# Kernel tuning notes

Hardware: AMD Instinct MI355X
Metric: run time of the kernel (lower is better)

The kernel has to match this reference:

```python
import jax, jax.numpy as jnp
import numpy as np

EPSILON = 0.1
GAMMA = 1.0
STOPERR = 1e-06
NUM_ITER_MAX = 1000


def setup_inputs() -> dict:
    key = jax.random.key(0)
    P = jax.random.uniform(key, (65536, 1024), dtype=jnp.float32)
    return {"P": P}


def _sinkhorn_scalings(Q, Pa, Pb, fi):
    # Iterate b <- (Pb / (Q^T a))^fi with a = Pa / (Q b); device-side convergence check.
    K = Q.shape[1]
    b0 = jnp.full((K, 1), 1.0 / K, dtype=Q.dtype)
    a0 = jnp.zeros((Q.shape[0], 1), dtype=Q.dtype)  # overwritten on first iter

    def cond(state):
        a, b, err, it = state
        return jnp.logical_and(err > STOPERR, it < NUM_ITER_MAX)

    def body(state):
        _, b, _, it = state
        a = Pa / jnp.maximum(Q @ b, 1e-12)            # (N,1)
        b_new = (Pb / jnp.maximum(Q.T @ a, 1e-12)) ** fi  # (K,1)
        err = jnp.linalg.norm(b_new - b)
        return (a, b_new, err, it + 1)

    a, b, _, _ = jax.lax.while_loop(
        cond, body, (a0, b0, jnp.float32(1.0), jnp.int32(0)))
    return a, b


def reference(P):
    N, K = P.shape
    eps = max(EPSILON, 1e-08)
    Q = jnp.maximum(jnp.exp(-P / eps), 1e-12)          # (N,K)
    Pa = jnp.full((N, 1), 1.0 / N, dtype=P.dtype)
    Pb = jnp.full((K, 1), 1.0 / K, dtype=P.dtype)
    fi = GAMMA / (GAMMA + eps)

    a, b = _sinkhorn_scalings(Q, Pa, Pb, fi)

    OT_plan = N * a * Q * b.T                          # (N,K)
    ot_loss = jnp.mean(jnp.sum(OT_plan * P, axis=1))
    w = jnp.mean(OT_plan, axis=0, keepdims=True)       # (1,K)
    w = w / (jnp.sum(w, axis=1, keepdims=True) + 1e-08)
    # F.kl_div(log(w+1e-7), Pb_row, reduction='batchmean'), batch size = 1:
    Pb_row = Pb.reshape(1, -1)
    reg = jnp.sum(Pb_row * (jnp.log(Pb_row) - jnp.log(w + 1e-07)))
    return (OT_plan, ot_loss, reg)
```

## Files before the change

### kernel.cpp

```cpp
#include <hip/hip_runtime.h>
#include <hip/hip_cooperative_groups.h>

constexpr int   NROWS = 65536;
constexpr int   NK    = 1024;
constexpr float PAv   = 1.0f / 65536.0f;
constexpr float PBv   = 1.0f / 1024.0f;
constexpr float FI    = 1.0f / 1.1f;
constexpr float NEG_INV_EPS = -10.0f;
constexpr float STOPERR2 = 1e-12f;
constexpr int   MAXIT = 1000;
constexpr float INVS  = 1.0f / 65535.0f;

__global__ __launch_bounds__(256)
void q_conv_kernel(const float* __restrict__ P, uint4* __restrict__ Qb)
{
  const size_t total8 = (size_t)NROWS * NK / 8;
  for (size_t i = (size_t)blockIdx.x * blockDim.x + threadIdx.x; i < total8;
       i += (size_t)gridDim.x * blockDim.x) {
    const float4* p4 = reinterpret_cast<const float4*>(P) + 2 * i;
    float4 a = p4[0], b = p4[1];
    unsigned int u0 = __float2uint_rn(__expf(a.x * NEG_INV_EPS) * 65535.0f);
    unsigned int u1 = __float2uint_rn(__expf(a.y * NEG_INV_EPS) * 65535.0f);
    unsigned int u2 = __float2uint_rn(__expf(a.z * NEG_INV_EPS) * 65535.0f);
    unsigned int u3 = __float2uint_rn(__expf(a.w * NEG_INV_EPS) * 65535.0f);
    unsigned int u4 = __float2uint_rn(__expf(b.x * NEG_INV_EPS) * 65535.0f);
    unsigned int u5 = __float2uint_rn(__expf(b.y * NEG_INV_EPS) * 65535.0f);
    unsigned int u6 = __float2uint_rn(__expf(b.z * NEG_INV_EPS) * 65535.0f);
    unsigned int u7 = __float2uint_rn(__expf(b.w * NEG_INV_EPS) * 65535.0f);
    uint4 o;
    o.x = u0 | (u1 << 16);
    o.y = u2 | (u3 << 16);
    o.z = u4 | (u5 << 16);
    o.w = u6 | (u7 << 16);
    Qb[i] = o;
  }
}

__device__ __forceinline__ unsigned long long pack2f(float a, float b) {
  return (unsigned long long)__float_as_uint(a) |
         ((unsigned long long)__float_as_uint(b) << 32);
}
__device__ __forceinline__ float lo2f(unsigned long long u) {
  return __uint_as_float((unsigned int)(u & 0xffffffffull));
}
__device__ __forceinline__ float hi2f(unsigned long long u) {
  return __uint_as_float((unsigned int)(u >> 32));
}

constexpr int IT_BLOCKS  = 256;
constexpr int IT_THREADS = 512;
constexpr int IT_WAVES   = IT_THREADS / 64;
constexpr int IT_RPW     = NROWS / (IT_BLOCKS * IT_WAVES);
constexpr int NCTR       = 16;
constexpr int CTR_STRIDE = 64;

template<bool U16>
__global__ __launch_bounds__(IT_THREADS, 2)
void ssk_iter(const void* __restrict__ src,
              unsigned long long* __restrict__ partial ,
              unsigned long long* __restrict__ bvec    ,
              unsigned int* __restrict__ ctrs          ,
              float* __restrict__ b_out)
{
  __shared__ float b_lds[NK];
  __shared__ float wave_cs[IT_WAVES][NK];
  __shared__ float redsh[IT_WAVES];
  __shared__ float fred[4][4];
  __shared__ float err_sh;

  const int tid  = threadIdx.x;
  const int wave = tid >> 6;
  const int lane = tid & 63;
  const int bid  = blockIdx.x;
  const int row0 = (bid * IT_WAVES + wave) * IT_RPW;

  b_lds[tid] = PBv; b_lds[tid + 512] = PBv;
  __syncthreads();

  int it = 0;
  int ph = 0;
  for (;;) {
    float bb[16];
    #pragma unroll
    for (int k = 0; k < 4; ++k)
      #pragma unroll
      for (int j = 0; j < 4; ++j)
        bb[4 * k + j] = b_lds[256 * k + 4 * lane + j];

    float acc[16];
    #pragma unroll
    for (int t = 0; t < 16; ++t) acc[t] = 0.0f;

    for (int r = 0; r < IT_RPW; r += 2) {
      float4 va[4], vb[4];
      if constexpr (U16) {
        const uint2* rA = reinterpret_cast<const uint2*>(src)
                        + (size_t)(row0 + r) * (NK / 4);
        const uint2* rB = rA + (NK / 4);
        uint2 ua[4], ub[4];
        #pragma unroll
        for (int k = 0; k < 4; ++k) { ua[k] = rA[(k << 6) + lane]; ub[k] = rB[(k << 6) + lane]; }
        #pragma unroll
        for (int k = 0; k < 4; ++k) {
          va[k].x = (float)(ua[k].x & 0xffffu) * INVS;
          va[k].y = (float)(ua[k].x >> 16)     * INVS;
          va[k].z = (float)(ua[k].y & 0xffffu) * INVS;
          va[k].w = (float)(ua[k].y >> 16)     * INVS;
          vb[k].x = (float)(ub[k].x & 0xffffu) * INVS;
          vb[k].y = (float)(ub[k].x >> 16)     * INVS;
          vb[k].z = (float)(ub[k].y & 0xffffu) * INVS;
          vb[k].w = (float)(ub[k].y >> 16)     * INVS;
        }
      } else {
        const float4* rpA = reinterpret_cast<const float4*>(src) + (size_t)(row0 + r)     * (NK / 4);
        const float4* rpB = reinterpret_cast<const float4*>(src) + (size_t)(row0 + r + 1) * (NK / 4);
        #pragma unroll
        for (int k = 0; k < 4; ++k) { va[k] = rpA[(k << 6) + lane]; vb[k] = rpB[(k << 6) + lane]; }
        #pragma unroll
        for (int k = 0; k < 4; ++k) {
          va[k].x = __expf(va[k].x * NEG_INV_EPS);
          va[k].y = __expf(va[k].y * NEG_INV_EPS);
          va[k].z = __expf(va[k].z * NEG_INV_EPS);
          va[k].w = __expf(va[k].w * NEG_INV_EPS);
          vb[k].x = __expf(vb[k].x * NEG_INV_EPS);
          vb[k].y = __expf(vb[k].y * NEG_INV_EPS);
          vb[k].z = __expf(vb[k].z * NEG_INV_EPS);
          vb[k].w = __expf(vb[k].w * NEG_INV_EPS);
        }
      }
      float dA = 0.f, dB = 0.f;
      #pragma unroll
      for (int k = 0; k < 4; ++k) {
        dA = fmaf(va[k].x, bb[4*k+0], dA);
        dA = fmaf(va[k].y, bb[4*k+1], dA);
        dA = fmaf(va[k].z, bb[4*k+2], dA);
        dA = fmaf(va[k].w, bb[4*k+3], dA);
        dB = fmaf(vb[k].x, bb[4*k+0], dB);
        dB = fmaf(vb[k].y, bb[4*k+1], dB);
        dB = fmaf(vb[k].z, bb[4*k+2], dB);
        dB = fmaf(vb[k].w, bb[4*k+3], dB);
      }
      #pragma unroll
      for (int off = 32; off; off >>= 1) {
        dA += __shfl_xor(dA, off);
        dB += __shfl_xor(dB, off);
      }
      const float aA = PAv / fmaxf(dA, 1e-12f);
      const float aB = PAv / fmaxf(dB, 1e-12f);
      #pragma unroll
      for (int k = 0; k < 4; ++k) {
        acc[4*k+0] = fmaf(aA, va[k].x, acc[4*k+0]);
        acc[4*k+1] = fmaf(aA, va[k].y, acc[4*k+1]);
        acc[4*k+2] = fmaf(aA, va[k].z, acc[4*k+2]);
        acc[4*k+3] = fmaf(aA, va[k].w, acc[4*k+3]);
        acc[4*k+0] = fmaf(aB, vb[k].x, acc[4*k+0]);
        acc[4*k+1] = fmaf(aB, vb[k].y, acc[4*k+1]);
        acc[4*k+2] = fmaf(aB, vb[k].z, acc[4*k+2]);
        acc[4*k+3] = fmaf(aB, vb[k].w, acc[4*k+3]);
      }
    }

    #pragma unroll
    for (int k = 0; k < 4; ++k)
      #pragma unroll
      for (int j = 0; j < 4; ++j)
        wave_cs[wave][256 * k + 4 * lane + j] = acc[4 * k + j];
    __syncthreads();

    {
      const int c0i = 2 * tid, c1i = 2 * tid + 1;
      float s0 = 0.f, s1 = 0.f;
      #pragma unroll
      for (int w = 0; w < IT_WAVES; ++w) { s0 += wave_cs[w][c0i]; s1 += wave_cs[w][c1i]; }
      __hip_atomic_store(&partial[bid * 512 + tid], pack2f(s0, s1),
                         __ATOMIC_RELAXED, __HIP_MEMORY_SCOPE_AGENT);
    }

    ++ph;
    __builtin_amdgcn_fence(__ATOMIC_RELEASE, "agent");
    __syncthreads();
    if (tid == 0)
      __hip_atomic_fetch_add(&ctrs[(bid & (NCTR - 1)) * CTR_STRIDE], 1u,
                             __ATOMIC_RELAXED, __HIP_MEMORY_SCOPE_AGENT);
    if (tid < NCTR) {
      const unsigned int tgt = (unsigned int)ph * (IT_BLOCKS / NCTR);
      while (__hip_atomic_load(&ctrs[tid * CTR_STRIDE], __ATOMIC_RELAXED,
                               __HIP_MEMORY_SCOPE_AGENT) < tgt)
        __builtin_amdgcn_s_sleep(4);
    }
    __syncthreads();
    asm volatile("" ::: "memory");

    if (tid < 256) {
      unsigned long long u0 = __hip_atomic_load(&partial[tid * 512 + 2 * bid],
                                                __ATOMIC_RELAXED, __HIP_MEMORY_SCOPE_AGENT);
      unsigned long long u1 = __hip_atomic_load(&partial[tid * 512 + 2 * bid + 1],
                                                __ATOMIC_RELAXED, __HIP_MEMORY_SCOPE_AGENT);
      float v0 = lo2f(u0), v1 = hi2f(u0), v2 = lo2f(u1), v3 = hi2f(u1);
      #pragma unroll
      for (int off = 32; off; off >>= 1) {
        v0 += __shfl_xor(v0, off);
        v1 += __shfl_xor(v1, off);
        v2 += __shfl_xor(v2, off);
        v3 += __shfl_xor(v3, off);
      }
      if (lane == 0) { fred[wave][0] = v0; fred[wave][1] = v1; fred[wave][2] = v2; fred[wave][3] = v3; }
    }
    __syncthreads();
    if (tid == 0) {
      float c0 = fred[0][0] + fred[1][0] + fred[2][0] + fred[3][0];
      float c1 = fred[0][1] + fred[1][1] + fred[2][1] + fred[3][1];
      float c2 = fred[0][2] + fred[1][2] + fred[2][2] + fred[3][2];
      float c3 = fred[0][3] + fred[1][3] + fred[2][3] + fred[3][3];
      const float b0 = powf(PBv / fmaxf(c0, 1e-12f), FI);
      const float b1 = powf(PBv / fmaxf(c1, 1e-12f), FI);
      const float b2 = powf(PBv / fmaxf(c2, 1e-12f), FI);
      const float b3 = powf(PBv / fmaxf(c3, 1e-12f), FI);
      __hip_atomic_store(&bvec[2 * bid],     pack2f(b0, b1),
                         __ATOMIC_RELAXED, __HIP_MEMORY_SCOPE_AGENT);
      __hip_atomic_store(&bvec[2 * bid + 1], pack2f(b2, b3),
                         __ATOMIC_RELAXED, __HIP_MEMORY_SCOPE_AGENT);
    }

    ++ph;
    __builtin_amdgcn_fence(__ATOMIC_RELEASE, "agent");
    __syncthreads();
    if (tid == 0)
      __hip_atomic_fetch_add(&ctrs[(bid & (NCTR - 1)) * CTR_STRIDE], 1u,
                             __ATOMIC_RELAXED, __HIP_MEMORY_SCOPE_AGENT);
    if (tid < NCTR) {
      const unsigned int tgt = (unsigned int)ph * (IT_BLOCKS / NCTR);
      while (__hip_atomic_load(&ctrs[tid * CTR_STRIDE], __ATOMIC_RELAXED,
                               __HIP_MEMORY_SCOPE_AGENT) < tgt)
        __builtin_amdgcn_s_sleep(4);
    }
    __syncthreads();
    asm volatile("" ::: "memory");

    const unsigned long long ub = __hip_atomic_load(&bvec[tid], __ATOMIC_RELAXED,
                                                    __HIP_MEMORY_SCOPE_AGENT);
    const float bn0 = lo2f(ub), bn1 = hi2f(ub);
    const float o0 = b_lds[2 * tid], o1 = b_lds[2 * tid + 1];
    const float e0 = bn0 - o0, e1 = bn1 - o1;
    float sq = e0 * e0 + e1 * e1;
    #pragma unroll
    for (int off = 32; off; off >>= 1) sq += __shfl_xor(sq, off);
    if (lane == 0) redsh[wave] = sq;
    __syncthreads();
    if (tid == 0) {
      float s = 0.f;
      #pragma unroll
      for (int w = 0; w < IT_WAVES; ++w) s += redsh[w];
      err_sh = s;
    }
    b_lds[2 * tid] = bn0; b_lds[2 * tid + 1] = bn1;
    ++it;
    __syncthreads();
    if (err_sh <= STOPERR2 || it >= MAXIT) break;
  }

  if (blockIdx.x == 0) { b_out[tid] = b_lds[tid]; b_out[tid + 512] = b_lds[tid + 512]; }
}

constexpr int FN_BLOCKS  = 2048;
constexpr int FN_THREADS = 256;
constexpr int FN_WAVES   = FN_THREADS / 64;
constexpr int FN_RPW     = NROWS / (FN_BLOCKS * FN_WAVES);

__global__ __launch_bounds__(FN_THREADS)
void ssk_finalize_kernel(const float* __restrict__ P, const float* __restrict__ b_glob,
                         float* __restrict__ out, float* __restrict__ wsum,
                         float* __restrict__ loss_part)
{
  __shared__ float b_sh[NK];
  __shared__ float wave_w[FN_WAVES][NK];
  __shared__ float red[FN_WAVES];

  const int tid  = threadIdx.x;
  const int wave = tid >> 6;
  const int lane = tid & 63;

  #pragma unroll
  for (int i = 0; i < 4; ++i) b_sh[tid + 256 * i] = b_glob[tid + 256 * i];
  __syncthreads();

  float bb[16];
  #pragma unroll
  for (int k = 0; k < 4; ++k)
    #pragma unroll
    for (int j = 0; j < 4; ++j)
      bb[4 * k + j] = b_sh[256 * k + 4 * lane + j];

  float wacc[16];
  #pragma unroll
  for (int t = 0; t < 16; ++t) wacc[t] = 0.0f;
  float lacc = 0.0f;

  const int row0 = (blockIdx.x * FN_WAVES + wave) * FN_RPW;
  float4* out4 = reinterpret_cast<float4*>(out);

  for (int r = 0; r < FN_RPW; ++r) {
    const size_t row = (size_t)(row0 + r);
    const float4* rp = reinterpret_cast<const float4*>(P) + row * (NK / 4);
    float4 pv[4];
    float Q[16];
    float dot = 0.0f;
    #pragma unroll
    for (int k = 0; k < 4; ++k) {
      pv[k] = rp[(k << 6) + lane];
      Q[4*k+0] = __expf(pv[k].x * NEG_INV_EPS);
      Q[4*k+1] = __expf(pv[k].y * NEG_INV_EPS);
      Q[4*k+2] = __expf(pv[k].z * NEG_INV_EPS);
      Q[4*k+3] = __expf(pv[k].w * NEG_INV_EPS);
      dot = fmaf(Q[4*k+0], bb[4*k+0], dot);
      dot = fmaf(Q[4*k+1], bb[4*k+1], dot);
      dot = fmaf(Q[4*k+2], bb[4*k+2], dot);
      dot = fmaf(Q[4*k+3], bb[4*k+3], dot);
    }
    #pragma unroll
    for (int off = 32; off; off >>= 1) dot += __shfl_xor(dot, off);
    const float s = 1.0f / fmaxf(dot, 1e-12f);
    #pragma unroll
    for (int k = 0; k < 4; ++k) {
      float4 o;
      o.x = s * Q[4*k+0] * bb[4*k+0];
      o.y = s * Q[4*k+1] * bb[4*k+1];
      o.z = s * Q[4*k+2] * bb[4*k+2];
      o.w = s * Q[4*k+3] * bb[4*k+3];
      out4[row * (NK / 4) + (k << 6) + lane] = o;
      lacc = fmaf(o.x, pv[k].x, lacc);
      lacc = fmaf(o.y, pv[k].y, lacc);
      lacc = fmaf(o.z, pv[k].z, lacc);
      lacc = fmaf(o.w, pv[k].w, lacc);
      wacc[4*k+0] += o.x; wacc[4*k+1] += o.y; wacc[4*k+2] += o.z; wacc[4*k+3] += o.w;
    }
  }

  #pragma unroll
  for (int k = 0; k < 4; ++k)
    #pragma unroll
    for (int j = 0; j < 4; ++j)
      wave_w[wave][256 * k + 4 * lane + j] = wacc[4 * k + j];
  __syncthreads();
  #pragma unroll
  for (int i = 0; i < 4; ++i) {
    const int c = tid + 256 * i;
    float s2 = wave_w[0][c] + wave_w[1][c] + wave_w[2][c] + wave_w[3][c];
    atomicAdd(&wsum[c], s2);
  }

  #pragma unroll
  for (int off = 32; off; off >>= 1) lacc += __shfl_xor(lacc, off);
  if (lane == 0) red[wave] = lacc;
  __syncthreads();
  if (tid == 0) loss_part[blockIdx.x] = red[0] + red[1] + red[2] + red[3];
}

__device__ __forceinline__ float ssk_block_sum_1024(float v, float* red, int wave, int lane)
{
  #pragma unroll
  for (int off = 32; off; off >>= 1) v += __shfl_xor(v, off);
  __syncthreads();
  if (lane == 0) red[wave] = v;
  __syncthreads();
  float t = 0.0f;
  #pragma unroll
  for (int w = 0; w < 16; ++w) t += red[w];
  return t;
}

__global__ __launch_bounds__(1024)
void ssk_finish_kernel(const float* __restrict__ wsum, const float* __restrict__ loss_part,
                       float* __restrict__ out)
{
  __shared__ float red[16];
  const int tid = threadIdx.x, wave = tid >> 6, lane = tid & 63;

  float l  = loss_part[tid] + loss_part[tid + 1024];
  float lt = ssk_block_sum_1024(l, red, wave, lane);

  float wm = wsum[tid] * (1.0f / (float)NROWS);
  float sw = ssk_block_sum_1024(wm, red, wave, lane);
  float wn = wm / (sw + 1e-8f);
  float v  = PBv * (logf(PBv) - logf(wn + 1e-7f));
  float rg = ssk_block_sum_1024(v, red, wave, lane);

  if (tid == 0) {
    out[(size_t)NROWS * NK]     = lt / (float)NROWS;
    out[(size_t)NROWS * NK + 1] = rg;
  }
}

extern "C" void kernel_launch(void* const* d_in, const int* in_sizes, int n_in,
                              void* d_out, int out_size, void* d_ws, size_t ws_size,
                              hipStream_t stream)
{
  const float* P = (const float*)d_in[0];
  float* out = (float*)d_out;
  float* ws  = (float*)d_ws;

  unsigned long long* partial = (unsigned long long*)d_out;
  unsigned long long* bvec    = (unsigned long long*)ws;
  unsigned int*       ctrs    = (unsigned int*)(ws + 1024);
  float* b_glob    = ws + 2048;
  float* wsum      = ws + 3072;
  float* loss_part = ws + 4096;

  const size_t QF   = (size_t)NROWS * NK / 2;
  const size_t need = (16384 + QF + 4096 + 2048) * sizeof(float);

  hipMemsetAsync(ws, 0, 4096 * sizeof(float), stream);

  if (ws_size >= need) {
    unsigned short* qbuf = (unsigned short*)(ws + 16384);
    q_conv_kernel<<<dim3(2048), dim3(256), 0, stream>>>(P, (uint4*)qbuf);

    const void* src = qbuf;
    void (*fp)(const void*, unsigned long long*, unsigned long long*,
               unsigned int*, float*) = ssk_iter<true>;
    void* args[] = { (void*)&src, (void*)&partial, (void*)&bvec, (void*)&ctrs,
                     (void*)&b_glob };
    hipLaunchCooperativeKernel((void*)fp, dim3(IT_BLOCKS), dim3(IT_THREADS),
                               args, 0, stream);
  } else {
    const void* src = (const void*)P;
    void (*fp)(const void*, unsigned long long*, unsigned long long*,
               unsigned int*, float*) = ssk_iter<false>;
    void* args[] = { (void*)&src, (void*)&partial, (void*)&bvec, (void*)&ctrs,
                     (void*)&b_glob };
    hipLaunchCooperativeKernel((void*)fp, dim3(IT_BLOCKS), dim3(IT_THREADS),
                               args, 0, stream);
  }

  ssk_finalize_kernel<<<dim3(FN_BLOCKS), dim3(FN_THREADS), 0, stream>>>(
      P, b_glob, out, wsum, loss_part);
  ssk_finish_kernel<<<dim3(1), dim3(1024), 0, stream>>>(wsum, loss_part, out);
}
```

Baseline: 11.52 ms.

## Double iteration block size and software-prefetch quantized Q rows across barriers

After: 17.94 ms. +55.8%, slower.

```diff
diff --git a/kernel.cpp b/kernel.cpp
--- a/kernel.cpp
+++ b/kernel.cpp
@@ -48,11 +48,23 @@
 }
 
 constexpr int IT_BLOCKS  = 256;
-constexpr int IT_THREADS = 512;
+constexpr int IT_THREADS = 1024;
 constexpr int IT_WAVES   = IT_THREADS / 64;
 constexpr int IT_RPW     = NROWS / (IT_BLOCKS * IT_WAVES);
 constexpr int NCTR       = 16;
 constexpr int CTR_STRIDE = 64;
+
+#define PREFETCH_BATCH(R)                                                     \
+  {                                                                           \
+    const uint2* rA_ = reinterpret_cast<const uint2*>(src)                    \
+                     + (size_t)(row0 + (R)) * (NK / 4);                       \
+    const uint2* rB_ = rA_ + (NK / 4);                                        \
+    _Pragma("unroll")                                                         \
+    for (int k = 0; k < 4; ++k) {                                             \
+      pa[k] = rA_[(k << 6) + lane];                                           \
+      pb[k] = rB_[(k << 6) + lane];                                           \
+    }                                                                         \
+  }
 
 template<bool U16>
 __global__ __launch_bounds__(IT_THREADS, 2)
@@ -74,8 +86,11 @@
   const int bid  = blockIdx.x;
   const int row0 = (bid * IT_WAVES + wave) * IT_RPW;
 
-  b_lds[tid] = PBv; b_lds[tid + 512] = PBv;
-  __syncthreads();
+  b_lds[tid] = PBv;
+  __syncthreads();
+
+  uint2 pa[4], pb[4];
+  if constexpr (U16) { PREFETCH_BATCH(0); }
 
   int it = 0;
   int ph = 0;
@@ -94,12 +109,10 @@
     for (int r = 0; r < IT_RPW; r += 2) {
       float4 va[4], vb[4];
       if constexpr (U16) {
-        const uint2* rA = reinterpret_cast<const uint2*>(src)
-                        + (size_t)(row0 + r) * (NK / 4);
-        const uint2* rB = rA + (NK / 4);
         uint2 ua[4], ub[4];
         #pragma unroll
-        for (int k = 0; k < 4; ++k) { ua[k] = rA[(k << 6) + lane]; ub[k] = rB[(k << 6) + lane]; }
+        for (int k = 0; k < 4; ++k) { ua[k] = pa[k]; ub[k] = pb[k]; }
+        if (r + 2 < IT_RPW) { PREFETCH_BATCH(r + 2); }
         #pragma unroll
         for (int k = 0; k < 4; ++k) {
           va[k].x = (float)(ua[k].x & 0xffffu) * INVS;
@@ -167,7 +180,7 @@
         wave_cs[wave][256 * k + 4 * lane + j] = acc[4 * k + j];
     __syncthreads();
 
-    {
+    if (tid < 512) {
       const int c0i = 2 * tid, c1i = 2 * tid + 1;
       float s0 = 0.f, s1 = 0.f;
       #pragma unroll
@@ -182,6 +195,7 @@
     if (tid == 0)
       __hip_atomic_fetch_add(&ctrs[(bid & (NCTR - 1)) * CTR_STRIDE], 1u,
                              __ATOMIC_RELAXED, __HIP_MEMORY_SCOPE_AGENT);
+    if constexpr (U16) { PREFETCH_BATCH(0); }
     if (tid < NCTR) {
       const unsigned int tgt = (unsigned int)ph * (IT_BLOCKS / NCTR);
       while (__hip_atomic_load(&ctrs[tid * CTR_STRIDE], __ATOMIC_RELAXED,
@@ -237,12 +251,16 @@
     __syncthreads();
     asm volatile("" ::: "memory");
 
-    const unsigned long long ub = __hip_atomic_load(&bvec[tid], __ATOMIC_RELAXED,
-                                                    __HIP_MEMORY_SCOPE_AGENT);
-    const float bn0 = lo2f(ub), bn1 = hi2f(ub);
-    const float o0 = b_lds[2 * tid], o1 = b_lds[2 * tid + 1];
-    const float e0 = bn0 - o0, e1 = bn1 - o1;
-    float sq = e0 * e0 + e1 * e1;
+    float sq = 0.0f;
+    float bn0 = 0.f, bn1 = 0.f;
+    if (tid < 512) {
+      const unsigned long long ub = __hip_atomic_load(&bvec[tid], __ATOMIC_RELAXED,
+                                                      __HIP_MEMORY_SCOPE_AGENT);
+      bn0 = lo2f(ub); bn1 = hi2f(ub);
+      const float o0 = b_lds[2 * tid], o1 = b_lds[2 * tid + 1];
+      const float e0 = bn0 - o0, e1 = bn1 - o1;
+      sq = e0 * e0 + e1 * e1;
+    }
     #pragma unroll
     for (int off = 32; off; off >>= 1) sq += __shfl_xor(sq, off);
     if (lane == 0) redsh[wave] = sq;
@@ -253,13 +271,13 @@
       for (int w = 0; w < IT_WAVES; ++w) s += redsh[w];
       err_sh = s;
     }
-    b_lds[2 * tid] = bn0; b_lds[2 * tid + 1] = bn1;
+    if (tid < 512) { b_lds[2 * tid] = bn0; b_lds[2 * tid + 1] = bn1; }
     ++it;
     __syncthreads();
     if (err_sh <= STOPERR2 || it >= MAXIT) break;
   }
 
-  if (blockIdx.x == 0) { b_out[tid] = b_lds[tid]; b_out[tid + 512] = b_lds[tid + 512]; }
+  if (blockIdx.x == 0) b_out[tid] = b_lds[tid];
 }
 
 constexpr int FN_BLOCKS  = 2048;
```
